# Performance work log

Measured on AMD Instinct MI355X. Metric: run time of the kernel, lower is better.

The kernel has to match this reference:

```python
import jax, jax.numpy as jnp
import numpy as np

B, G, D = 2, 2048, 128
H, K, V = 8, 16, 16


def setup_inputs() -> dict:
    key = jax.random.key(0)
    k1, k2, k3, k4 = jax.random.split(key, 4)
    return {
        "h": jax.random.normal(k1, (B, G, D), dtype=jnp.float32),
        "W_Q": jax.random.normal(k2, (H, D, K), dtype=jnp.float32) / np.sqrt(D),
        "W_K": jax.random.normal(k3, (H, D, K), dtype=jnp.float32) / np.sqrt(D),
        "W_V": jax.random.normal(k4, (H, D, V), dtype=jnp.float32) / np.sqrt(D),
    }


def reference(h, W_Q, W_K, W_V):
    # h: [B, G, D]; per-head projections -> [B, H, G, K/V]
    compat_factor = 1.0 / np.sqrt(W_Q.shape[-1]).astype(np.float32)
    q = jnp.einsum("bgd,hdk->bhgk", h, W_Q)
    k = jnp.einsum("bgd,hdk->bhgk", h, W_K)
    v = jnp.einsum("bgd,hdv->bhgv", h, W_V)
    # compatibility: [B, H, G, G]
    compat = compat_factor * jnp.einsum("bhqk,bhmk->bhqm", q, k)
    attention = jax.nn.softmax(compat, axis=-1)
    # h_p: [B, H, G, V]
    h_p = jnp.einsum("bhqm,bhmv->bhqv", attention, v)
    return h_p
```

## Files before the change

kernel.cpp:

```cpp
#include <hip/hip_runtime.h>
#include <hip/hip_bf16.h>

constexpr int Gc = 2048, Dc = 128, Hc = 8, Kc = 16;
constexpr int NCT = 24;
constexpr int NCH = 128;
constexpr int SPLIT = 4;
constexpr int CPS = NCH / SPLIT;

typedef __attribute__((ext_vector_type(8))) short bf16x8;
typedef __attribute__((ext_vector_type(4))) unsigned short u16x4;
typedef __attribute__((ext_vector_type(8))) unsigned short u16x8;
typedef __attribute__((ext_vector_type(4))) float f32x4;

static __device__ __forceinline__ unsigned short f2bf(float f) {
  unsigned int u = __float_as_uint(f);
  u += 0x7FFFu + ((u >> 16) & 1u);
  return (unsigned short)(u >> 16);
}
static __device__ __forceinline__ float bf2f(unsigned short s) {
  return __uint_as_float(((unsigned int)s) << 16);
}
static __device__ __forceinline__ float fexp2(float x) {
#if __has_builtin(__builtin_amdgcn_exp2f)
  return __builtin_amdgcn_exp2f(x);
#else
  return exp2f(x);
#endif
}
static __device__ __forceinline__ unsigned int pk_bf16(float lo, float hi) {
  __hip_bfloat162 b = __float22bfloat162_rn(make_float2(lo, hi));
  union { __hip_bfloat162 b2; unsigned int u; } cvt;
  cvt.b2 = b;
  return cvt.u;
}

__global__ __launch_bounds__(256) void prep_kernel(
    const float* __restrict__ h, const float* __restrict__ Wq,
    const float* __restrict__ Wk, const float* __restrict__ Wv,
    unsigned short* __restrict__ hhi, unsigned short* __restrict__ hlo,
    unsigned short* __restrict__ WfH, unsigned short* __restrict__ WfL) {
  if (blockIdx.x < 512) {
    const int t = blockIdx.x * 256 + threadIdx.x;
    const float4 v = *(const float4*)(h + (size_t)t * 4);
    const float a[4] = {v.x, v.y, v.z, v.w};
    u16x4 hi, lo;
#pragma unroll
    for (int i = 0; i < 4; ++i) {
      const unsigned short hb = f2bf(a[i]);
      hi[i] = hb;
      lo[i] = f2bf(a[i] - bf2f(hb));
    }
    *(u16x4*)(hhi + (size_t)t * 4) = hi;
    *(u16x4*)(hlo + (size_t)t * 4) = lo;
  } else {
    const int t = (blockIdx.x - 512) * 256 + threadIdx.x;
    const int l = t & 63;
    const int kc = (t >> 6) & 3;
    const int ct = t >> 8;
    const int mat = ct >> 3, hh = ct & 7;
    const float* W = (mat == 0 ? Wq : (mat == 1 ? Wk : Wv)) + hh * (Dc * Kc);
    const float scale = (mat == 0) ? 0.25f * 1.44269504088896f : 1.0f;
    const int col = l & 15, g4 = l >> 4;
    u16x8 hi, lo;
#pragma unroll
    for (int j = 0; j < 8; ++j) {
      const int d = kc * 32 + g4 * 8 + j;
      const float w = W[d * Kc + col] * scale;
      const unsigned short hb = f2bf(w);
      hi[j] = hb;
      lo[j] = f2bf(w - bf2f(hb));
    }
    *(u16x8*)(WfH + (size_t)t * 8) = hi;
    *(u16x8*)(WfL + (size_t)t * 8) = lo;
  }
}

__global__ __launch_bounds__(256) void proj_gemm_kernel(
    const unsigned short* __restrict__ hhi, const unsigned short* __restrict__ hlo,
    const unsigned short* __restrict__ WfH, const unsigned short* __restrict__ WfL,
    float* __restrict__ Q, unsigned short* __restrict__ Khi,
    unsigned short* __restrict__ Klo, unsigned short* __restrict__ Vf) {
  const int widx = blockIdx.x * 4 + (threadIdx.x >> 6);
  const int ct = widx % NCT;
  const int rt = widx / NCT;
  const int l = threadIdx.x & 63;
  const int lane15 = l & 15, g4 = l >> 4;
  const int row0 = rt * 16;

  const unsigned short* ah_p = hhi + (size_t)(row0 + lane15) * Dc + g4 * 8;
  const unsigned short* al_p = hlo + (size_t)(row0 + lane15) * Dc + g4 * 8;
  const unsigned short* bh_p = WfH + (size_t)ct * 2048 + l * 8;
  const unsigned short* bl_p = WfL + (size_t)ct * 2048 + l * 8;

  f32x4 acc = {0.f, 0.f, 0.f, 0.f};
#pragma unroll
  for (int kc = 0; kc < 4; ++kc) {
    const bf16x8 ah = *(const bf16x8*)(ah_p + kc * 32);
    const bf16x8 al = *(const bf16x8*)(al_p + kc * 32);
    const bf16x8 bh = *(const bf16x8*)(bh_p + kc * 512);
    const bf16x8 bl = *(const bf16x8*)(bl_p + kc * 512);
    acc = __builtin_amdgcn_mfma_f32_16x16x32_bf16(ah, bh, acc, 0, 0, 0);
    acc = __builtin_amdgcn_mfma_f32_16x16x32_bf16(ah, bl, acc, 0, 0, 0);
    acc = __builtin_amdgcn_mfma_f32_16x16x32_bf16(al, bh, acc, 0, 0, 0);
  }

  const int mat = ct >> 3, hh = ct & 7;
  const int b = row0 >> 11;
  const int g0 = row0 & 2047;
  const int bhh = b * Hc + hh;
  if (mat == 0) {
#pragma unroll
    for (int i = 0; i < 4; ++i)
      Q[((size_t)bhh * Gc + g0 + g4 * 4 + i) * Kc + lane15] = acc[i];
  } else if (mat == 1) {
#pragma unroll
    for (int i = 0; i < 4; ++i) {
      const size_t off = ((size_t)bhh * Gc + g0 + g4 * 4 + i) * Kc + lane15;
      const unsigned short hb = f2bf(acc[i]);
      Khi[off] = hb;
      Klo[off] = f2bf(acc[i] - bf2f(hb));
    }
  } else {
    const int c = g0 >> 4;
    u16x8 fv;
#pragma unroll
    for (int i = 0; i < 4; ++i) {
      const unsigned short hb = f2bf(acc[i]);
      fv[i] = hb;
      fv[i + 4] = f2bf(acc[i] - bf2f(hb));
    }
    *(u16x8*)(Vf + ((size_t)(bhh * NCH + c) * 64 + l) * 8) = fv;
  }
}

__global__ __launch_bounds__(256) void flash_kernel(
    const float* __restrict__ Q, const unsigned short* __restrict__ Khi,
    const unsigned short* __restrict__ Klo, const unsigned short* __restrict__ Vf,
    float* __restrict__ part_o, float* __restrict__ part_ml) {
  const int gid = blockIdx.x * 4 + (threadIdx.x >> 6);
  const int split = gid & 3;
  const int qt = gid >> 2;
  const int bh = qt >> 7, qi = qt & 127;
  const int l = threadIdx.x & 63;
  const int lane15 = l & 15, g4 = l >> 4, dhalf = g4 & 1;

  const float* qp = Q + ((size_t)bh * Gc + qi * 16 + lane15) * Kc + 8 * dhalf;
  bf16x8 bqh, bql;
#pragma unroll
  for (int i = 0; i < 8; ++i) {
    const float x = qp[i];
    const unsigned short hb = f2bf(x);
    bqh[i] = (short)hb;
    bql[i] = (short)f2bf(x - bf2f(hb));
  }

  const unsigned short* kbase = (g4 >= 2 ? Klo : Khi) +
      (size_t)bh * Gc * Kc + lane15 * Kc + 8 * dhalf;
  const unsigned short* vf = Vf + ((size_t)bh * NCH * 64 + l) * 8;

  const int c0 = split * CPS, c1 = c0 + CPS;
  f32x4 o = {0.f, 0.f, 0.f, 0.f};
  float run_max = -1e30f, lsum = 0.f;

#pragma unroll 4
  for (int c = c0; c < c1; ++c) {
    const bf16x8 ak = *(const bf16x8*)(kbase + (size_t)c * 256);
    const bf16x8 av = *(const bf16x8*)(vf + (size_t)c * 512);

    f32x4 s = {0.f, 0.f, 0.f, 0.f};
    s = __builtin_amdgcn_mfma_f32_16x16x32_bf16(ak, bql, s, 0, 0, 0);
    s = __builtin_amdgcn_mfma_f32_16x16x32_bf16(ak, bqh, s, 0, 0, 0);

    const float cm = fmaxf(fmaxf(s[0], s[1]), fmaxf(s[2], s[3]));
    if (!__all((int)(cm - run_max <= 11.5f))) {
      float fm = fmaxf(cm, __shfl_xor(cm, 16));
      fm = fmaxf(fm, __shfl_xor(fm, 32));
      const float nm = fmaxf(run_max, fm);
      const float corr = fexp2(run_max - nm);
      o[0] *= corr; o[1] *= corr; o[2] *= corr; o[3] *= corr;
      lsum *= corr;
      run_max = nm;
    }
    const float p0 = fexp2(s[0] - run_max), p1 = fexp2(s[1] - run_max);
    const float p2 = fexp2(s[2] - run_max), p3 = fexp2(s[3] - run_max);
    lsum += (p0 + p1) + (p2 + p3);

    union { bf16x8 v; unsigned int w[4]; } bp;
    const unsigned int w01 = pk_bf16(p0, p1);
    const unsigned int w23 = pk_bf16(p2, p3);
    bp.w[0] = w01; bp.w[1] = w23; bp.w[2] = w01; bp.w[3] = w23;

    o = __builtin_amdgcn_mfma_f32_16x16x32_bf16(av, bp.v, o, 0, 0, 0);
  }

  float ls = lsum;
  ls += __shfl_xor(ls, 16);
  ls += __shfl_xor(ls, 32);

  const int pw = qt * SPLIT + split;
  *(f32x4*)(part_o + ((size_t)pw * 64 + l) * 4) = o;
  if (l < 16) {
    part_ml[pw * 32 + l * 2] = run_max;
    part_ml[pw * 32 + l * 2 + 1] = ls;
  }
}

__global__ __launch_bounds__(256) void combine_kernel(
    const float* __restrict__ part_o, const float* __restrict__ part_ml,
    float* __restrict__ out) {
  const int qt = blockIdx.x * 4 + (threadIdx.x >> 6);
  const int l = threadIdx.x & 63;
  const int lane15 = l & 15, g4 = l >> 4;
  const int pw0 = qt * SPLIT;

  float m[SPLIT], lv[SPLIT];
#pragma unroll
  for (int s = 0; s < SPLIT; ++s) {
    const float2 ml = *(const float2*)(part_ml + (pw0 + s) * 32 + lane15 * 2);
    m[s] = ml.x;
    lv[s] = ml.y;
  }
  const float M = fmaxf(fmaxf(m[0], m[1]), fmaxf(m[2], m[3]));
  f32x4 acc = {0.f, 0.f, 0.f, 0.f};
  float den = 0.f;
#pragma unroll
  for (int s = 0; s < SPLIT; ++s) {
    const float w = fexp2(m[s] - M);
    den += w * lv[s];
    const f32x4 po = *(const f32x4*)(part_o + ((size_t)(pw0 + s) * 64 + l) * 4);
    acc[0] += w * po[0]; acc[1] += w * po[1];
    acc[2] += w * po[2]; acc[3] += w * po[3];
  }
  const float inv = 1.0f / den;
  f32x4 res;
  res[0] = acc[0] * inv; res[1] = acc[1] * inv;
  res[2] = acc[2] * inv; res[3] = acc[3] * inv;
  const int bh = qt >> 7, qi = qt & 127;
  *(f32x4*)(out + ((size_t)bh * Gc + qi * 16 + lane15) * Kc + 4 * g4) = res;
}

extern "C" void kernel_launch(void* const* d_in, const int* in_sizes, int n_in,
                              void* d_out, int out_size, void* d_ws, size_t ws_size,
                              hipStream_t stream) {
  const float* h  = (const float*)d_in[0];
  const float* Wq = (const float*)d_in[1];
  const float* Wk = (const float*)d_in[2];
  const float* Wv = (const float*)d_in[3];
  float* out = (float*)d_out;

  char* ws = (char*)d_ws;
  float* Q            = (float*)(ws);
  unsigned short* Khi = (unsigned short*)(ws + (2u << 20));
  unsigned short* Klo = (unsigned short*)(ws + (3u << 20));
  unsigned short* Vf  = (unsigned short*)(ws + (4u << 20));
  unsigned short* hhi = (unsigned short*)(ws + (6u << 20));
  unsigned short* hlo = (unsigned short*)(ws + (7u << 20));
  unsigned short* WfH = (unsigned short*)(ws + (8u << 20));
  unsigned short* WfL = (unsigned short*)(ws + (8u << 20) + (1u << 18));
  float* part_o  = (float*)(ws + (9u << 20));
  float* part_ml = (float*)(ws + (17u << 20));

  prep_kernel<<<536, 256, 0, stream>>>(h, Wq, Wk, Wv, hhi, hlo, WfH, WfL);
  proj_gemm_kernel<<<1536, 256, 0, stream>>>(hhi, hlo, WfH, WfL, Q, Khi, Klo, Vf);
  flash_kernel<<<2048, 256, 0, stream>>>(Q, Khi, Klo, Vf, part_o, part_ml);
  combine_kernel<<<512, 256, 0, stream>>>(part_o, part_ml, out);
}
```

Measured before the change: 102.4 us.

## Fuse split-K combine into flash kernel via shared memory and process two chunks per iteration

The four KV-split partial results for a query tile now sit in one workgroup, one wave per split, and are merged through shared memory. This removes the separate combine kernel launch and the global round trip of the partial outputs. The main loop also handles two key chunks per iteration with two independent accumulators, which gives more MFMA work to overlap. The rescale check now compares against a cached threshold, which drops a subtraction each iteration. In exchange the kernel gains a __syncthreads and more register pressure, and one wave does the final merge while the other three sit idle.

```diff
diff --git a/kernel.cpp b/kernel.cpp
--- a/kernel.cpp
+++ b/kernel.cpp
@@ -136,10 +136,12 @@
 __global__ __launch_bounds__(256) void flash_kernel(
     const float* __restrict__ Q, const unsigned short* __restrict__ Khi,
     const unsigned short* __restrict__ Klo, const unsigned short* __restrict__ Vf,
-    float* __restrict__ part_o, float* __restrict__ part_ml) {
-  const int gid = blockIdx.x * 4 + (threadIdx.x >> 6);
-  const int split = gid & 3;
-  const int qt = gid >> 2;
+    float* __restrict__ out) {
+  __shared__ f32x4 lo_s[SPLIT][64];
+  __shared__ float lml[SPLIT][16][2];
+
+  const int qt = blockIdx.x;
+  const int split = threadIdx.x >> 6;
   const int bh = qt >> 7, qi = qt & 127;
   const int l = threadIdx.x & 63;
   const int lane15 = l & 15, g4 = l >> 4, dhalf = g4 & 1;
@@ -158,85 +160,91 @@
       (size_t)bh * Gc * Kc + lane15 * Kc + 8 * dhalf;
   const unsigned short* vf = Vf + ((size_t)bh * NCH * 64 + l) * 8;
 
-  const int c0 = split * CPS, c1 = c0 + CPS;
-  f32x4 o = {0.f, 0.f, 0.f, 0.f};
-  float run_max = -1e30f, lsum = 0.f;
-
-#pragma unroll 4
-  for (int c = c0; c < c1; ++c) {
-    const bf16x8 ak = *(const bf16x8*)(kbase + (size_t)c * 256);
-    const bf16x8 av = *(const bf16x8*)(vf + (size_t)c * 512);
-
-    f32x4 s = {0.f, 0.f, 0.f, 0.f};
-    s = __builtin_amdgcn_mfma_f32_16x16x32_bf16(ak, bql, s, 0, 0, 0);
-    s = __builtin_amdgcn_mfma_f32_16x16x32_bf16(ak, bqh, s, 0, 0, 0);
-
-    const float cm = fmaxf(fmaxf(s[0], s[1]), fmaxf(s[2], s[3]));
-    if (!__all((int)(cm - run_max <= 11.5f))) {
+  const int c0 = split * CPS;
+  const f32x4 z = {0.f, 0.f, 0.f, 0.f};
+  f32x4 o0 = z, o1 = z;
+  float run_max = -1e30f, thr = -1e30f, lsum = 0.f;
+
+#pragma unroll 2
+  for (int it = 0; it < CPS / 2; ++it) {
+    const int c = c0 + it * 2;
+    const bf16x8 ak0 = *(const bf16x8*)(kbase + (size_t)c * 256);
+    const bf16x8 ak1 = *(const bf16x8*)(kbase + (size_t)c * 256 + 256);
+    const bf16x8 av0 = *(const bf16x8*)(vf + (size_t)c * 512);
+    const bf16x8 av1 = *(const bf16x8*)(vf + (size_t)c * 512 + 512);
+
+    f32x4 s0 = __builtin_amdgcn_mfma_f32_16x16x32_bf16(ak0, bql, z, 0, 0, 0);
+    s0 = __builtin_amdgcn_mfma_f32_16x16x32_bf16(ak0, bqh, s0, 0, 0, 0);
+    f32x4 s1 = __builtin_amdgcn_mfma_f32_16x16x32_bf16(ak1, bql, z, 0, 0, 0);
+    s1 = __builtin_amdgcn_mfma_f32_16x16x32_bf16(ak1, bqh, s1, 0, 0, 0);
+
+    const float cm = fmaxf(fmaxf(fmaxf(s0[0], s0[1]), fmaxf(s0[2], s0[3])),
+                           fmaxf(fmaxf(s1[0], s1[1]), fmaxf(s1[2], s1[3])));
+    if (!__all((int)(cm <= thr))) {
       float fm = fmaxf(cm, __shfl_xor(cm, 16));
       fm = fmaxf(fm, __shfl_xor(fm, 32));
       const float nm = fmaxf(run_max, fm);
       const float corr = fexp2(run_max - nm);
-      o[0] *= corr; o[1] *= corr; o[2] *= corr; o[3] *= corr;
+      o0[0] *= corr; o0[1] *= corr; o0[2] *= corr; o0[3] *= corr;
+      o1[0] *= corr; o1[1] *= corr; o1[2] *= corr; o1[3] *= corr;
       lsum *= corr;
       run_max = nm;
-    }
-    const float p0 = fexp2(s[0] - run_max), p1 = fexp2(s[1] - run_max);
-    const float p2 = fexp2(s[2] - run_max), p3 = fexp2(s[3] - run_max);
-    lsum += (p0 + p1) + (p2 + p3);
-
-    union { bf16x8 v; unsigned int w[4]; } bp;
-    const unsigned int w01 = pk_bf16(p0, p1);
-    const unsigned int w23 = pk_bf16(p2, p3);
-    bp.w[0] = w01; bp.w[1] = w23; bp.w[2] = w01; bp.w[3] = w23;
-
-    o = __builtin_amdgcn_mfma_f32_16x16x32_bf16(av, bp.v, o, 0, 0, 0);
-  }
-
+      thr = nm + 11.5f;
+    }
+    const float p0 = fexp2(s0[0] - run_max), p1 = fexp2(s0[1] - run_max);
+    const float p2 = fexp2(s0[2] - run_max), p3 = fexp2(s0[3] - run_max);
+    const float p4 = fexp2(s1[0] - run_max), p5 = fexp2(s1[1] - run_max);
+    const float p6 = fexp2(s1[2] - run_max), p7 = fexp2(s1[3] - run_max);
+    lsum += ((p0 + p1) + (p2 + p3)) + ((p4 + p5) + (p6 + p7));
+
+    union { bf16x8 v; unsigned int w[4]; } bp0, bp1;
+    const unsigned int a01 = pk_bf16(p0, p1), a23 = pk_bf16(p2, p3);
+    const unsigned int b01 = pk_bf16(p4, p5), b23 = pk_bf16(p6, p7);
+    bp0.w[0] = a01; bp0.w[1] = a23; bp0.w[2] = a01; bp0.w[3] = a23;
+    bp1.w[0] = b01; bp1.w[1] = b23; bp1.w[2] = b01; bp1.w[3] = b23;
+
+    o0 = __builtin_amdgcn_mfma_f32_16x16x32_bf16(av0, bp0.v, o0, 0, 0, 0);
+    o1 = __builtin_amdgcn_mfma_f32_16x16x32_bf16(av1, bp1.v, o1, 0, 0, 0);
+  }
+
+  f32x4 o;
+  o[0] = o0[0] + o1[0]; o[1] = o0[1] + o1[1];
+  o[2] = o0[2] + o1[2]; o[3] = o0[3] + o1[3];
   float ls = lsum;
   ls += __shfl_xor(ls, 16);
   ls += __shfl_xor(ls, 32);
 
-  const int pw = qt * SPLIT + split;
-  *(f32x4*)(part_o + ((size_t)pw * 64 + l) * 4) = o;
+  lo_s[split][l] = o;
   if (l < 16) {
-    part_ml[pw * 32 + l * 2] = run_max;
-    part_ml[pw * 32 + l * 2 + 1] = ls;
-  }
-}
-
-__global__ __launch_bounds__(256) void combine_kernel(
-    const float* __restrict__ part_o, const float* __restrict__ part_ml,
-    float* __restrict__ out) {
-  const int qt = blockIdx.x * 4 + (threadIdx.x >> 6);
-  const int l = threadIdx.x & 63;
-  const int lane15 = l & 15, g4 = l >> 4;
-  const int pw0 = qt * SPLIT;
-
-  float m[SPLIT], lv[SPLIT];
-#pragma unroll
-  for (int s = 0; s < SPLIT; ++s) {
-    const float2 ml = *(const float2*)(part_ml + (pw0 + s) * 32 + lane15 * 2);
-    m[s] = ml.x;
-    lv[s] = ml.y;
-  }
-  const float M = fmaxf(fmaxf(m[0], m[1]), fmaxf(m[2], m[3]));
-  f32x4 acc = {0.f, 0.f, 0.f, 0.f};
-  float den = 0.f;
-#pragma unroll
-  for (int s = 0; s < SPLIT; ++s) {
-    const float w = fexp2(m[s] - M);
-    den += w * lv[s];
-    const f32x4 po = *(const f32x4*)(part_o + ((size_t)(pw0 + s) * 64 + l) * 4);
-    acc[0] += w * po[0]; acc[1] += w * po[1];
-    acc[2] += w * po[2]; acc[3] += w * po[3];
-  }
-  const float inv = 1.0f / den;
-  f32x4 res;
-  res[0] = acc[0] * inv; res[1] = acc[1] * inv;
-  res[2] = acc[2] * inv; res[3] = acc[3] * inv;
-  const int bh = qt >> 7, qi = qt & 127;
-  *(f32x4*)(out + ((size_t)bh * Gc + qi * 16 + lane15) * Kc + 4 * g4) = res;
+    lml[split][l][0] = run_max;
+    lml[split][l][1] = ls;
+  }
+  __syncthreads();
+
+  if (threadIdx.x < 64) {
+    float m[SPLIT], lv[SPLIT];
+#pragma unroll
+    for (int s = 0; s < SPLIT; ++s) {
+      m[s] = lml[s][lane15][0];
+      lv[s] = lml[s][lane15][1];
+    }
+    const float M = fmaxf(fmaxf(m[0], m[1]), fmaxf(m[2], m[3]));
+    f32x4 acc = {0.f, 0.f, 0.f, 0.f};
+    float den = 0.f;
+#pragma unroll
+    for (int s = 0; s < SPLIT; ++s) {
+      const float w = fexp2(m[s] - M);
+      den += w * lv[s];
+      const f32x4 po = lo_s[s][l];
+      acc[0] += w * po[0]; acc[1] += w * po[1];
+      acc[2] += w * po[2]; acc[3] += w * po[3];
+    }
+    const float inv = 1.0f / den;
+    f32x4 res;
+    res[0] = acc[0] * inv; res[1] = acc[1] * inv;
+    res[2] = acc[2] * inv; res[3] = acc[3] * inv;
+    *(f32x4*)(out + ((size_t)bh * Gc + qi * 16 + lane15) * Kc + 4 * g4) = res;
+  }
 }
 
 extern "C" void kernel_launch(void* const* d_in, const int* in_sizes, int n_in,
@@ -257,11 +265,8 @@
   unsigned short* hlo = (unsigned short*)(ws + (7u << 20));
   unsigned short* WfH = (unsigned short*)(ws + (8u << 20));
   unsigned short* WfL = (unsigned short*)(ws + (8u << 20) + (1u << 18));
-  float* part_o  = (float*)(ws + (9u << 20));
-  float* part_ml = (float*)(ws + (17u << 20));
 
   prep_kernel<<<536, 256, 0, stream>>>(h, Wq, Wk, Wv, hhi, hlo, WfH, WfL);
   proj_gemm_kernel<<<1536, 256, 0, stream>>>(hhi, hlo, WfH, WfL, Q, Khi, Klo, Vf);
-  flash_kernel<<<2048, 256, 0, stream>>>(Q, Khi, Klo, Vf, part_o, part_ml);
-  combine_kernel<<<512, 256, 0, stream>>>(part_o, part_ml, out);
-}
+  flash_kernel<<<2048, 256, 0, stream>>>(Q, Khi, Klo, Vf, out);
+}
```

New measurement: 99.78 us. -2.5%, faster.

## Fuse split-KV combine into flash kernel via shared memory, two q-tiles per wave

Applied to the files above, without the earlier changes.

The separate combine kernel is removed. Each 512-thread block now runs 8 KV splits as waves over two query tiles and merges the partial softmax results through shared memory before writing the output. This drops a kernel launch and the global round trip for the partial O, max and sum values. Each K/V chunk load is reused across two query tiles, and the rescale threshold is precomputed. In exchange there is more register pressure, a block-wide barrier, and only 2 of the 8 waves do the final combine.

```diff
diff --git a/kernel.cpp b/kernel.cpp
--- a/kernel.cpp
+++ b/kernel.cpp
@@ -4,7 +4,8 @@
 constexpr int Gc = 2048, Dc = 128, Hc = 8, Kc = 16;
 constexpr int NCT = 24;
 constexpr int NCH = 128;
-constexpr int SPLIT = 4;
+constexpr int SPLIT = 8;
+constexpr int QPW = 2;
 constexpr int CPS = NCH / SPLIT;
 
 typedef __attribute__((ext_vector_type(8))) short bf16x8;
@@ -133,110 +134,121 @@
   }
 }
 
-__global__ __launch_bounds__(256) void flash_kernel(
+__global__ __launch_bounds__(512) void flash_kernel(
     const float* __restrict__ Q, const unsigned short* __restrict__ Khi,
     const unsigned short* __restrict__ Klo, const unsigned short* __restrict__ Vf,
-    float* __restrict__ part_o, float* __restrict__ part_ml) {
-  const int gid = blockIdx.x * 4 + (threadIdx.x >> 6);
-  const int split = gid & 3;
-  const int qt = gid >> 2;
-  const int bh = qt >> 7, qi = qt & 127;
+    float* __restrict__ out) {
+  __shared__ f32x4 lo_s[SPLIT][QPW][64];
+  __shared__ float lml[SPLIT][QPW][16][2];
+
+  const int qg = blockIdx.x;
+  const int split = threadIdx.x >> 6;
+  const int bh = qg >> 6;
+  const int qi0 = (qg & 63) * QPW;
   const int l = threadIdx.x & 63;
   const int lane15 = l & 15, g4 = l >> 4, dhalf = g4 & 1;
 
-  const float* qp = Q + ((size_t)bh * Gc + qi * 16 + lane15) * Kc + 8 * dhalf;
-  bf16x8 bqh, bql;
-#pragma unroll
-  for (int i = 0; i < 8; ++i) {
-    const float x = qp[i];
-    const unsigned short hb = f2bf(x);
-    bqh[i] = (short)hb;
-    bql[i] = (short)f2bf(x - bf2f(hb));
+  bf16x8 bqh[QPW], bql[QPW];
+#pragma unroll
+  for (int t = 0; t < QPW; ++t) {
+    const float* qp =
+        Q + ((size_t)bh * Gc + (qi0 + t) * 16 + lane15) * Kc + 8 * dhalf;
+#pragma unroll
+    for (int i = 0; i < 8; ++i) {
+      const float x = qp[i];
+      const unsigned short hb = f2bf(x);
+      bqh[t][i] = (short)hb;
+      bql[t][i] = (short)f2bf(x - bf2f(hb));
+    }
   }
 
   const unsigned short* kbase = (g4 >= 2 ? Klo : Khi) +
       (size_t)bh * Gc * Kc + lane15 * Kc + 8 * dhalf;
   const unsigned short* vf = Vf + ((size_t)bh * NCH * 64 + l) * 8;
 
-  const int c0 = split * CPS, c1 = c0 + CPS;
-  f32x4 o = {0.f, 0.f, 0.f, 0.f};
-  float run_max = -1e30f, lsum = 0.f;
-
-#pragma unroll 4
-  for (int c = c0; c < c1; ++c) {
+  const int c0 = split * CPS;
+  const f32x4 z = {0.f, 0.f, 0.f, 0.f};
+  f32x4 o[QPW] = {z, z};
+  float run_max[QPW] = {-1e30f, -1e30f};
+  float thr[QPW] = {-1e30f, -1e30f};
+  float lsum[QPW] = {0.f, 0.f};
+
+  for (int c = c0; c < c0 + CPS; ++c) {
     const bf16x8 ak = *(const bf16x8*)(kbase + (size_t)c * 256);
     const bf16x8 av = *(const bf16x8*)(vf + (size_t)c * 512);
 
-    f32x4 s = {0.f, 0.f, 0.f, 0.f};
-    s = __builtin_amdgcn_mfma_f32_16x16x32_bf16(ak, bql, s, 0, 0, 0);
-    s = __builtin_amdgcn_mfma_f32_16x16x32_bf16(ak, bqh, s, 0, 0, 0);
-
-    const float cm = fmaxf(fmaxf(s[0], s[1]), fmaxf(s[2], s[3]));
-    if (!__all((int)(cm - run_max <= 11.5f))) {
-      float fm = fmaxf(cm, __shfl_xor(cm, 16));
-      fm = fmaxf(fm, __shfl_xor(fm, 32));
-      const float nm = fmaxf(run_max, fm);
-      const float corr = fexp2(run_max - nm);
-      o[0] *= corr; o[1] *= corr; o[2] *= corr; o[3] *= corr;
-      lsum *= corr;
-      run_max = nm;
-    }
-    const float p0 = fexp2(s[0] - run_max), p1 = fexp2(s[1] - run_max);
-    const float p2 = fexp2(s[2] - run_max), p3 = fexp2(s[3] - run_max);
-    lsum += (p0 + p1) + (p2 + p3);
-
-    union { bf16x8 v; unsigned int w[4]; } bp;
-    const unsigned int w01 = pk_bf16(p0, p1);
-    const unsigned int w23 = pk_bf16(p2, p3);
-    bp.w[0] = w01; bp.w[1] = w23; bp.w[2] = w01; bp.w[3] = w23;
-
-    o = __builtin_amdgcn_mfma_f32_16x16x32_bf16(av, bp.v, o, 0, 0, 0);
-  }
-
-  float ls = lsum;
-  ls += __shfl_xor(ls, 16);
-  ls += __shfl_xor(ls, 32);
-
-  const int pw = qt * SPLIT + split;
-  *(f32x4*)(part_o + ((size_t)pw * 64 + l) * 4) = o;
-  if (l < 16) {
-    part_ml[pw * 32 + l * 2] = run_max;
-    part_ml[pw * 32 + l * 2 + 1] = ls;
-  }
-}
-
-__global__ __launch_bounds__(256) void combine_kernel(
-    const float* __restrict__ part_o, const float* __restrict__ part_ml,
-    float* __restrict__ out) {
-  const int qt = blockIdx.x * 4 + (threadIdx.x >> 6);
-  const int l = threadIdx.x & 63;
-  const int lane15 = l & 15, g4 = l >> 4;
-  const int pw0 = qt * SPLIT;
-
-  float m[SPLIT], lv[SPLIT];
-#pragma unroll
-  for (int s = 0; s < SPLIT; ++s) {
-    const float2 ml = *(const float2*)(part_ml + (pw0 + s) * 32 + lane15 * 2);
-    m[s] = ml.x;
-    lv[s] = ml.y;
-  }
-  const float M = fmaxf(fmaxf(m[0], m[1]), fmaxf(m[2], m[3]));
-  f32x4 acc = {0.f, 0.f, 0.f, 0.f};
-  float den = 0.f;
-#pragma unroll
-  for (int s = 0; s < SPLIT; ++s) {
-    const float w = fexp2(m[s] - M);
-    den += w * lv[s];
-    const f32x4 po = *(const f32x4*)(part_o + ((size_t)(pw0 + s) * 64 + l) * 4);
-    acc[0] += w * po[0]; acc[1] += w * po[1];
-    acc[2] += w * po[2]; acc[3] += w * po[3];
-  }
-  const float inv = 1.0f / den;
-  f32x4 res;
-  res[0] = acc[0] * inv; res[1] = acc[1] * inv;
-  res[2] = acc[2] * inv; res[3] = acc[3] * inv;
-  const int bh = qt >> 7, qi = qt & 127;
-  *(f32x4*)(out + ((size_t)bh * Gc + qi * 16 + lane15) * Kc + 4 * g4) = res;
+#pragma unroll
+    for (int t = 0; t < QPW; ++t) {
+      f32x4 s = __builtin_amdgcn_mfma_f32_16x16x32_bf16(ak, bql[t], z, 0, 0, 0);
+      s = __builtin_amdgcn_mfma_f32_16x16x32_bf16(ak, bqh[t], s, 0, 0, 0);
+
+      const float cm = fmaxf(fmaxf(s[0], s[1]), fmaxf(s[2], s[3]));
+      if (!__all((int)(cm <= thr[t]))) {
+        float fm = fmaxf(cm, __shfl_xor(cm, 16));
+        fm = fmaxf(fm, __shfl_xor(fm, 32));
+        const float nm = fmaxf(run_max[t], fm);
+        const float corr = fexp2(run_max[t] - nm);
+        o[t][0] *= corr; o[t][1] *= corr; o[t][2] *= corr; o[t][3] *= corr;
+        lsum[t] *= corr;
+        run_max[t] = nm;
+        thr[t] = nm + 11.5f;
+      }
+      const float p0 = fexp2(s[0] - run_max[t]);
+      const float p1 = fexp2(s[1] - run_max[t]);
+      const float p2 = fexp2(s[2] - run_max[t]);
+      const float p3 = fexp2(s[3] - run_max[t]);
+      lsum[t] += (p0 + p1) + (p2 + p3);
+
+      union { bf16x8 v; unsigned int w[4]; } bp;
+      const unsigned int w01 = pk_bf16(p0, p1);
+      const unsigned int w23 = pk_bf16(p2, p3);
+      bp.w[0] = w01; bp.w[1] = w23; bp.w[2] = w01; bp.w[3] = w23;
+
+      o[t] = __builtin_amdgcn_mfma_f32_16x16x32_bf16(av, bp.v, o[t], 0, 0, 0);
+    }
+  }
+
+#pragma unroll
+  for (int t = 0; t < QPW; ++t) {
+    float ls = lsum[t];
+    ls += __shfl_xor(ls, 16);
+    ls += __shfl_xor(ls, 32);
+    lo_s[split][t][l] = o[t];
+    if (l < 16) {
+      lml[split][t][l][0] = run_max[t];
+      lml[split][t][l][1] = ls;
+    }
+  }
+  __syncthreads();
+
+  if (threadIdx.x < QPW * 64) {
+    const int t = split;
+    float m[SPLIT], lv[SPLIT];
+#pragma unroll
+    for (int s = 0; s < SPLIT; ++s) {
+      m[s] = lml[s][t][lane15][0];
+      lv[s] = lml[s][t][lane15][1];
+    }
+    float M = m[0];
+#pragma unroll
+    for (int s = 1; s < SPLIT; ++s) M = fmaxf(M, m[s]);
+    f32x4 acc = {0.f, 0.f, 0.f, 0.f};
+    float den = 0.f;
+#pragma unroll
+    for (int s = 0; s < SPLIT; ++s) {
+      const float w = fexp2(m[s] - M);
+      den += w * lv[s];
+      const f32x4 po = lo_s[s][t][l];
+      acc[0] += w * po[0]; acc[1] += w * po[1];
+      acc[2] += w * po[2]; acc[3] += w * po[3];
+    }
+    const float inv = 1.0f / den;
+    f32x4 res;
+    res[0] = acc[0] * inv; res[1] = acc[1] * inv;
+    res[2] = acc[2] * inv; res[3] = acc[3] * inv;
+    *(f32x4*)(out + ((size_t)bh * Gc + (qi0 + t) * 16 + lane15) * Kc + 4 * g4) =
+        res;
+  }
 }
 
 extern "C" void kernel_launch(void* const* d_in, const int* in_sizes, int n_in,
@@ -257,11 +269,8 @@
   unsigned short* hlo = (unsigned short*)(ws + (7u << 20));
   unsigned short* WfH = (unsigned short*)(ws + (8u << 20));
   unsigned short* WfL = (unsigned short*)(ws + (8u << 20) + (1u << 18));
-  float* part_o  = (float*)(ws + (9u << 20));
-  float* part_ml = (float*)(ws + (17u << 20));
 
   prep_kernel<<<536, 256, 0, stream>>>(h, Wq, Wk, Wv, hhi, hlo, WfH, WfL);
   proj_gemm_kernel<<<1536, 256, 0, stream>>>(hhi, hlo, WfH, WfL, Q, Khi, Klo, Vf);
-  flash_kernel<<<2048, 256, 0, stream>>>(Q, Khi, Klo, Vf, part_o, part_ml);
-  combine_kernel<<<512, 256, 0, stream>>>(part_o, part_ml, out);
-}
+  flash_kernel<<<1024, 512, 0, stream>>>(Q, Khi, Klo, Vf, out);
+}
```

New measurement: 98.93 us. -3.4%, faster.
